# Kernel optimization log

Hardware: AMD Instinct MI355X
Metric: run time of the kernel (lower is better)

## Reference

```python
import jax, jax.numpy as jnp
import numpy as np

DIM = 128        # per-head dim == model width in this module
Q_HEADS = 16
KV_HEADS = 4
WINDOW = 512
BATCH = 4
SEQ = 2048


def setup_inputs() -> dict:
    key = jax.random.key(0)
    k1, k2, k3 = jax.random.split(key, 3)
    x = jax.random.normal(k1, (BATCH, SEQ, DIM), dtype=jnp.float32)
    # fused qkv weight, stored (in, out) so forward is x @ W_qkv
    W_qkv = jax.random.normal(k2, (DIM, (Q_HEADS + 2 * KV_HEADS) * DIM), dtype=jnp.float32) * (DIM ** -0.5)
    W_proj = jax.random.normal(k3, (Q_HEADS * DIM, DIM), dtype=jnp.float32) * ((Q_HEADS * DIM) ** -0.5)
    return {"x": x, "W_qkv": W_qkv, "W_proj": W_proj}


def _gqa_forward(x, W_qkv, W_proj):
    b, s, d = x.shape
    qkv = x @ W_qkv                                    # [b, s, (Hq+2Hkv)*d]
    qkv = qkv.reshape(b, s, Q_HEADS + 2 * KV_HEADS, d).transpose(0, 2, 1, 3)
    q = qkv[:, :Q_HEADS]                               # [b, Hq, s, d]
    k = qkv[:, Q_HEADS:Q_HEADS + KV_HEADS]             # [b, Hkv, s, d]
    v = qkv[:, Q_HEADS + KV_HEADS:]                    # [b, Hkv, s, d]

    # GQA: repeat kv heads to match q heads
    group = Q_HEADS // KV_HEADS
    k = jnp.repeat(k, group, axis=1)                   # [b, Hq, s, d]
    v = jnp.repeat(v, group, axis=1)

    scale = 1.0 / jnp.sqrt(jnp.float32(d))
    scores = jnp.einsum('bhqd,bhkd->bhqk', q, k) * scale   # [b, Hq, s, s]

    q_idx = jnp.arange(s)[:, None]
    kv_idx = jnp.arange(s)[None, :]
    rel = (q_idx - kv_idx).astype(jnp.float32)         # [s, s]
    # per-head ALiBi slope: exp2(-(h+1)*8/Hq), added (sign matches source)
    h = jnp.arange(Q_HEADS, dtype=jnp.float32)
    slopes = jnp.exp2(-((h + 1.0) * 8.0 / Q_HEADS))    # [Hq]
    scores = scores + slopes[None, :, None, None] * rel[None, None, :, :]

    mask = (q_idx >= kv_idx) & ((q_idx - kv_idx) <= WINDOW)
    scores = jnp.where(mask[None, None], scores, -jnp.inf)
    probs = jax.nn.softmax(scores, axis=-1)

    att = jnp.einsum('bhqk,bhkd->bhqd', probs, v)      # [b, Hq, s, d]
    att = att.transpose(0, 2, 1, 3).reshape(b, s, Q_HEADS * d)
    return att @ W_proj                                # [b, s, d]


def reference(x, W_qkv, W_proj):
    return _gqa_forward(x, W_qkv, W_proj)
```

## Files before the change

kernel.cpp:

```cpp
#include <hip/hip_runtime.h>
#include <math.h>

#define DIM_    128
#define QH_     16
#define KVH_    4
#define WIN_    512
#define BATCH_  4
#define SEQ_    2048
#define QKV_LD  3072
#define ATT_LD  2048

#define NX   (BATCH_*SEQ_*DIM_)
#define NWQ  (DIM_*QKV_LD)
#define NWP  (ATT_LD*DIM_)

typedef __attribute__((ext_vector_type(8))) short short8;
typedef __attribute__((ext_vector_type(4))) float f32x4;
typedef unsigned short u16;
typedef unsigned int u32;

__device__ __forceinline__ u16 f2bf(float f) {
    u32 u = __float_as_uint(f);
    u += 0x7fff + ((u >> 16) & 1);
    return (u16)(u >> 16);
}
__device__ __forceinline__ float bf2f(u16 u) {
    return __uint_as_float(((u32)u) << 16);
}
#define MFMA16 __builtin_amdgcn_mfma_f32_16x16x32_bf16

#if __has_builtin(__builtin_amdgcn_exp2f)
#define EXP2F __builtin_amdgcn_exp2f
#else
#define EXP2F exp2f
#endif

__device__ __forceinline__ void gload_lds16(const u16* g, u16* l) {
    __builtin_amdgcn_global_load_lds(
        (const __attribute__((address_space(1))) unsigned int*)(const void*)g,
        (__attribute__((address_space(3))) unsigned int*)(void*)l, 16, 0, 0);
}

__global__ __launch_bounds__(256) void prep(
    const float* __restrict__ x, const float* __restrict__ Wqkv,
    const float* __restrict__ Wproj,
    u16* __restrict__ xh, u16* __restrict__ wth, u16* __restrict__ wpth)
{
    if (blockIdx.x < 1024) {
        const size_t t = (size_t)blockIdx.x * 256 + threadIdx.x;
        float4 v = *(const float4*)(x + 4 * t);
        ushort4 o;
        o.x = f2bf(v.x); o.y = f2bf(v.y); o.z = f2bf(v.z); o.w = f2bf(v.w);
        *(ushort4*)(xh + 4 * t) = o;
        return;
    }
    __shared__ float T[32][33];
    int tile = blockIdx.x - 1024;
    const float* src; u16* dst; int K, N;
    if (tile < 384) { src = Wqkv;  dst = wth;  K = 128;  N = 3072; }
    else { tile -= 384; src = Wproj; dst = wpth; K = 2048; N = 128; }
    const int ntile = N >> 5;
    const int k0 = (tile / ntile) << 5, n0 = (tile % ntile) << 5;
    const int tx = threadIdx.x & 31, ty = threadIdx.x >> 5;
    #pragma unroll
    for (int i = 0; i < 4; ++i)
        T[ty + 8 * i][tx] = src[(size_t)(k0 + ty + 8 * i) * N + n0 + tx];
    __syncthreads();
    #pragma unroll
    for (int i = 0; i < 4; ++i)
        dst[(size_t)(n0 + ty + 8 * i) * K + k0 + tx] = f2bf(T[tx][ty + 8 * i]);
}

__global__ __launch_bounds__(256) void gemm1_mfma(
    const u16* __restrict__ xh, const u16* __restrict__ wth,
    u16* __restrict__ qkvb, u16* __restrict__ vg)
{
    __shared__ u16 Ab[32][512];
    __shared__ u16 Bb[16][512];
    const int bn = blockIdx.x * 64;
    const int bm = blockIdx.y * 128;
    const int tid = threadIdx.x;
    const int wv = tid >> 6, lane = tid & 63;
    const int lr = lane & 15, quad = lane >> 4;
    const int lo = lane & 15, hi = lane >> 4;

    #pragma unroll
    for (int i = 0; i < 12; ++i) {
        const int idx = wv * 12 + i;
        if (idx < 32) {
            const int mt = idx >> 2, s = idx & 3;
            gload_lds16(xh + (size_t)(bm + mt * 16 + lo) * DIM_ + s * 32 + hi * 8,
                        &Ab[idx][0]);
        } else {
            const int j = idx - 32, nt = j >> 2, s = j & 3;
            gload_lds16(wth + (size_t)(bn + nt * 16 + lo) * DIM_ + s * 32 + hi * 8,
                        &Bb[j][0]);
        }
    }
    __syncthreads();

    const int wr = wv >> 1, wc = wv & 1;
    f32x4 acc[4][2] = {};
    if (bn < 2560) {
        #pragma unroll
        for (int s = 0; s < 4; ++s) {
            short8 af[4], bf[2];
            #pragma unroll
            for (int mt = 0; mt < 4; ++mt)
                af[mt] = *(const short8*)&Ab[(wr * 4 + mt) * 4 + s][lane * 8];
            #pragma unroll
            for (int nt = 0; nt < 2; ++nt)
                bf[nt] = *(const short8*)&Bb[(wc * 2 + nt) * 4 + s][lane * 8];
            #pragma unroll
            for (int mt = 0; mt < 4; ++mt)
                #pragma unroll
                for (int nt = 0; nt < 2; ++nt)
                    acc[mt][nt] = MFMA16(bf[nt], af[mt], acc[mt][nt], 0, 0, 0);
        }
        #pragma unroll
        for (int mt = 0; mt < 4; ++mt)
            #pragma unroll
            for (int nt = 0; nt < 2; ++nt) {
                ushort4 o;
                o.x = f2bf(acc[mt][nt][0]); o.y = f2bf(acc[mt][nt][1]);
                o.z = f2bf(acc[mt][nt][2]); o.w = f2bf(acc[mt][nt][3]);
                *(ushort4*)(qkvb
                    + (size_t)(bm + wr * 64 + mt * 16 + lr) * QKV_LD
                    + bn + wc * 32 + nt * 16 + quad * 4) = o;
            }
    } else {
        #pragma unroll
        for (int s = 0; s < 4; ++s) {
            short8 af[4], bf[2];
            #pragma unroll
            for (int mt = 0; mt < 4; ++mt)
                af[mt] = *(const short8*)&Ab[(wr * 4 + mt) * 4 + s][lane * 8];
            #pragma unroll
            for (int nt = 0; nt < 2; ++nt)
                bf[nt] = *(const short8*)&Bb[(wc * 2 + nt) * 4 + s][lane * 8];
            #pragma unroll
            for (int mt = 0; mt < 4; ++mt)
                #pragma unroll
                for (int nt = 0; nt < 2; ++nt)
                    acc[mt][nt] = MFMA16(af[mt], bf[nt], acc[mt][nt], 0, 0, 0);
        }
        #pragma unroll
        for (int mt = 0; mt < 4; ++mt)
            #pragma unroll
            for (int nt = 0; nt < 2; ++nt) {
                const int ncol = bn + wc * 32 + nt * 16 + lr - 2560;
                const int kvh = ncol >> 7, d = ncol & 127;
                const int m0 = bm + wr * 64 + mt * 16 + quad * 4;
                ushort4 o;
                o.x = f2bf(acc[mt][nt][0]); o.y = f2bf(acc[mt][nt][1]);
                o.z = f2bf(acc[mt][nt][2]); o.w = f2bf(acc[mt][nt][3]);
                *(ushort4*)(vg + ((size_t)((m0 >> 11) * KVH_ + kvh) * DIM_ + d)
                            * SEQ_ + (m0 & 2047)) = o;
            }
    }
}

__global__ __launch_bounds__(256) void attn_mfma(
    const u16* __restrict__ qkvb, const u16* __restrict__ vg,
    u16* __restrict__ ah)
{
    const int xcd  = blockIdx.x & 7;
    const int idx  = blockIdx.x >> 3;
    const int pair = xcd + 8 * (idx & 1);
    const int qt   = idx >> 1;
    const int b    = pair >> 2, kvh = pair & 3;
    const int q0 = qt << 5;
    const int tid = threadIdx.x;
    const int wv = tid >> 6, lane = tid & 63;
    const int lr = lane & 15, quad = lane >> 4;
    const int h = kvh * 4 + wv;

    __shared__ u16 Kb[4][8][512];
    __shared__ u16 Vb[4][8][512];
    __shared__ u16 Pt[4][32][36];

    const float scale2 = 0.08838834764831845f * 1.4426950408889634f;
    const float slope2 = exp2f(-0.5f * (float)(h + 1)) * 1.4426950408889634f;
    const int jbase = max(0, q0 - WIN_);
    const int nch = (q0 + 32 - jbase) >> 5;
    const size_t rowb = (size_t)b * SEQ_;
    const u16* kg  = qkvb + rowb * QKV_LD + (QH_ + kvh) * DIM_;
    const u16* vgb = vg + (size_t)(b * KVH_ + kvh) * DIM_ * SEQ_;
    const int lo = lane & 15, hi = lane >> 4;

    short8 qf[2][4];
    #pragma unroll
    for (int m = 0; m < 2; ++m) {
        const u16* qp = qkvb + (rowb + q0 + m * 16 + lr) * QKV_LD
                        + h * DIM_ + quad * 8;
        #pragma unroll
        for (int s = 0; s < 4; ++s) qf[m][s] = *(const short8*)(qp + 32 * s);
    }

    float alpha[2];
    #pragma unroll
    for (int m = 0; m < 2; ++m) {
        const int q = q0 + m * 16 + lr;
        const int rm = (q < WIN_) ? q : WIN_;
        alpha[m] = slope2 * (float)(q - rm);
    }

    f32x4 O[2][8] = {};
    float rs[2] = {0.f, 0.f};

    #define STAGE(CH, SLOT) do {                                              \
        const int _jk = jbase + ((CH) << 5);                                  \
        _Pragma("unroll")                                                     \
        for (int _t = 0; _t < 2; ++_t) {                                      \
            const int _p = wv + _t * 4;                                       \
            gload_lds16(kg + (size_t)(_jk + (_p >> 2) * 16 + lo) * QKV_LD     \
                        + (_p & 3) * 32 + hi * 8, &Kb[(SLOT)][_p][0]);        \
            gload_lds16(vgb + (size_t)(_p * 16 + lo) * SEQ_ + _jk + hi * 8,   \
                        &Vb[(SLOT)][_p][0]);                                  \
        }                                                                     \
    } while (0)

    STAGE(0, 0);
    { const int c1 = (1 < nch) ? 1 : (nch - 1); STAGE(c1, 1); }

    for (int ch = 0; ch < nch; ++ch) {
        const int jk = jbase + (ch << 5);
        const int slot = ch & 3;
        { const int cn = (ch + 2 < nch) ? (ch + 2) : (nch - 1);
          STAGE(cn, (ch + 2) & 3); }
        __asm__ volatile("s_waitcnt vmcnt(8)" ::: "memory");
        __asm__ volatile("s_barrier" ::: "memory");

        #pragma unroll
        for (int nt = 0; nt < 2; ++nt) {
            f32x4 c0 = {0.f, 0.f, 0.f, 0.f}, c1 = {0.f, 0.f, 0.f, 0.f};
            #pragma unroll
            for (int s = 0; s < 4; ++s) {
                short8 kf = *(const short8*)&Kb[slot][nt * 4 + s][lane * 8];
                c0 = MFMA16(kf, qf[0][s], c0, 0, 0, 0);
                c1 = MFMA16(kf, qf[1][s], c1, 0, 0, 0);
            }
            const int jknt = jk + nt * 16;
            #pragma unroll
            for (int m = 0; m < 2; ++m) {
                const f32x4 c = m ? c1 : c0;
                const int qm0 = q0 + m * 16;
                const float b0 = fmaf(-slope2, (float)(jknt + quad * 4), alpha[m]);
                float e0, e1, e2, e3;
                if (qm0 >= jknt + 15 && qm0 + 15 <= jknt + WIN_) {
                    e0 = EXP2F(fmaf(c[0], scale2, b0));
                    e1 = EXP2F(fmaf(c[1], scale2, b0 - slope2));
                    e2 = EXP2F(fmaf(c[2], scale2, b0 - 2.f * slope2));
                    e3 = EXP2F(fmaf(c[3], scale2, b0 - 3.f * slope2));
                } else {
                    const int q = qm0 + lr, j0q = jknt + quad * 4;
                    float ee[4];
                    #pragma unroll
                    for (int r = 0; r < 4; ++r) {
                        const int rel = q - (j0q + r);
                        const float t = fmaf(c[r], scale2, b0 - (float)r * slope2);
                        ee[r] = ((unsigned)rel <= (unsigned)WIN_) ? EXP2F(t) : 0.f;
                    }
                    e0 = ee[0]; e1 = ee[1]; e2 = ee[2]; e3 = ee[3];
                }
                rs[m] += (e0 + e1) + (e2 + e3);
                ushort4 o;
                o.x = f2bf(e0); o.y = f2bf(e1); o.z = f2bf(e2); o.w = f2bf(e3);
                *(ushort4*)&Pt[wv][m * 16 + lr][nt * 16 + quad * 4] = o;
            }
        }
        __asm__ volatile("s_waitcnt lgkmcnt(0)" ::: "memory");

        short8 pa0 = *(const short8*)&Pt[wv][lr][quad * 8];
        short8 pa1 = *(const short8*)&Pt[wv][16 + lr][quad * 8];
        #pragma unroll
        for (int nt = 0; nt < 8; ++nt) {
            short8 vf = *(const short8*)&Vb[slot][nt][lane * 8];
            O[0][nt] = MFMA16(vf, pa0, O[0][nt], 0, 0, 0);
            O[1][nt] = MFMA16(vf, pa1, O[1][nt], 0, 0, 0);
        }
    }
    #undef STAGE

    __asm__ volatile("s_waitcnt vmcnt(0)" ::: "memory");

    #pragma unroll
    for (int m = 0; m < 2; ++m) {
        rs[m] += __shfl_xor(rs[m], 16);
        rs[m] += __shfl_xor(rs[m], 32);
    }

    #pragma unroll
    for (int m = 0; m < 2; ++m) {
        const float inv = 1.0f / rs[m];
        u16* dst = ah + (rowb + q0 + m * 16 + lr) * (size_t)ATT_LD + h * DIM_;
        #pragma unroll
        for (int nt = 0; nt < 8; ++nt) {
            ushort4 o;
            o.x = f2bf(O[m][nt][0] * inv); o.y = f2bf(O[m][nt][1] * inv);
            o.z = f2bf(O[m][nt][2] * inv); o.w = f2bf(O[m][nt][3] * inv);
            *(ushort4*)(dst + nt * 16 + quad * 4) = o;
        }
    }
}

__global__ __launch_bounds__(256) void gemm2_mfma(
    const u16* __restrict__ ah, const u16* __restrict__ wpth,
    float* __restrict__ out)
{
    const int bm = blockIdx.x * 16;
    const int wv = threadIdx.x >> 6, lane = threadIdx.x & 63;
    const int lr = lane & 15, quad = lane >> 4;
    const int cq = wv;

    const u16* arow  = ah + (size_t)(bm + lr) * ATT_LD + quad * 8;
    const u16* w0row = wpth + (size_t)(cq * 32 + lr) * ATT_LD + quad * 8;
    const u16* w1row = w0row + (size_t)16 * ATT_LD;

    f32x4 acc0 = {0.f, 0.f, 0.f, 0.f}, acc1 = {0.f, 0.f, 0.f, 0.f};
    #pragma unroll 8
    for (int k0 = 0; k0 < ATT_LD; k0 += 32) {
        short8 a  = *(const short8*)(arow + k0);
        short8 w0 = *(const short8*)(w0row + k0);
        short8 w1 = *(const short8*)(w1row + k0);
        acc0 = MFMA16(w0, a, acc0, 0, 0, 0);
        acc1 = MFMA16(w1, a, acc1, 0, 0, 0);
    }
    float* orow = out + (size_t)(bm + lr) * DIM_ + cq * 32;
    *(float4*)(orow + quad * 4)      = *(float4*)&acc0;
    *(float4*)(orow + 16 + quad * 4) = *(float4*)&acc1;
}

extern "C" void kernel_launch(void* const* d_in, const int* in_sizes, int n_in,
                              void* d_out, int out_size, void* d_ws, size_t ws_size,
                              hipStream_t stream)
{
    const float* x     = (const float*)d_in[0];
    const float* Wqkv  = (const float*)d_in[1];
    const float* Wproj = (const float*)d_in[2];
    float* out = (float*)d_out;

    u16* xh   = (u16*)d_ws;
    u16* wth  = xh   + (size_t)NX;
    u16* wpth = wth  + (size_t)NWQ;
    u16* qkvb = wpth + (size_t)NWP;
    u16* vg   = qkvb + (size_t)8192 * QKV_LD;
    u16* ahp  = vg   + (size_t)BATCH_ * KVH_ * DIM_ * SEQ_;

    prep<<<1024 + 640, 256, 0, stream>>>(x, Wqkv, Wproj, xh, wth, wpth);

    gemm1_mfma<<<dim3(QKV_LD / 64, 8192 / 128), 256, 0, stream>>>(
        xh, wth, qkvb, vg);

    attn_mfma<<<1024, 256, 0, stream>>>(qkvb, vg, ahp);

    gemm2_mfma<<<8192 / 16, 256, 0, stream>>>(ahp, wpth, out);
}
```

Measured before the change: 202.0 us.

## Halve attention query tile, double-buffer K/V, use packed bf16 conversion

Cuts the attention query tile from 32 to 16 rows per wave and doubles the grid, so there are more blocks and fewer registers and less LDS per block. The K/V pipeline drops from four-slot depth-two prefetch to two-slot depth-one prefetch, adds a second barrier per chunk and clamps the last chunk's load address. Every fp32-to-bf16 conversion in the GEMM epilogue and attention now uses the hardware packed conversion instruction instead of manual rounding. The trade-off is that each K/V chunk is now loaded for only 16 query rows, which doubles K/V traffic, and load latency is less hidden.

```diff
diff --git a/kernel.cpp b/kernel.cpp
--- a/kernel.cpp
+++ b/kernel.cpp
@@ -26,6 +26,11 @@
 }
 __device__ __forceinline__ float bf2f(u16 u) {
     return __uint_as_float(((u32)u) << 16);
+}
+__device__ __forceinline__ u32 pkbf(float a, float b) {
+    u32 r;
+    __asm__("v_cvt_pk_bf16_f32 %0, %1, %2" : "=v"(r) : "v"(a), "v"(b));
+    return r;
 }
 #define MFMA16 __builtin_amdgcn_mfma_f32_16x16x32_bf16
 
@@ -121,10 +126,10 @@
         for (int mt = 0; mt < 4; ++mt)
             #pragma unroll
             for (int nt = 0; nt < 2; ++nt) {
-                ushort4 o;
-                o.x = f2bf(acc[mt][nt][0]); o.y = f2bf(acc[mt][nt][1]);
-                o.z = f2bf(acc[mt][nt][2]); o.w = f2bf(acc[mt][nt][3]);
-                *(ushort4*)(qkvb
+                uint2 o;
+                o.x = pkbf(acc[mt][nt][0], acc[mt][nt][1]);
+                o.y = pkbf(acc[mt][nt][2], acc[mt][nt][3]);
+                *(uint2*)(qkvb
                     + (size_t)(bm + wr * 64 + mt * 16 + lr) * QKV_LD
                     + bn + wc * 32 + nt * 16 + quad * 4) = o;
             }
@@ -151,16 +156,16 @@
                 const int ncol = bn + wc * 32 + nt * 16 + lr - 2560;
                 const int kvh = ncol >> 7, d = ncol & 127;
                 const int m0 = bm + wr * 64 + mt * 16 + quad * 4;
-                ushort4 o;
-                o.x = f2bf(acc[mt][nt][0]); o.y = f2bf(acc[mt][nt][1]);
-                o.z = f2bf(acc[mt][nt][2]); o.w = f2bf(acc[mt][nt][3]);
-                *(ushort4*)(vg + ((size_t)((m0 >> 11) * KVH_ + kvh) * DIM_ + d)
+                uint2 o;
+                o.x = pkbf(acc[mt][nt][0], acc[mt][nt][1]);
+                o.y = pkbf(acc[mt][nt][2], acc[mt][nt][3]);
+                *(uint2*)(vg + ((size_t)((m0 >> 11) * KVH_ + kvh) * DIM_ + d)
                             * SEQ_ + (m0 & 2047)) = o;
             }
     }
 }
 
-__global__ __launch_bounds__(256) void attn_mfma(
+__global__ __launch_bounds__(256, 4) void attn_mfma(
     const u16* __restrict__ qkvb, const u16* __restrict__ vg,
     u16* __restrict__ ah)
 {
@@ -169,47 +174,45 @@
     const int pair = xcd + 8 * (idx & 1);
     const int qt   = idx >> 1;
     const int b    = pair >> 2, kvh = pair & 3;
-    const int q0 = qt << 5;
+    const int q0 = qt << 4;
     const int tid = threadIdx.x;
     const int wv = tid >> 6, lane = tid & 63;
     const int lr = lane & 15, quad = lane >> 4;
     const int h = kvh * 4 + wv;
 
-    __shared__ u16 Kb[4][8][512];
-    __shared__ u16 Vb[4][8][512];
-    __shared__ u16 Pt[4][32][36];
+    __shared__ u16 Kb[2][8][512];
+    __shared__ u16 Vb[2][8][512];
+    __shared__ u16 Pt[4][16][36];
 
     const float scale2 = 0.08838834764831845f * 1.4426950408889634f;
     const float slope2 = exp2f(-0.5f * (float)(h + 1)) * 1.4426950408889634f;
     const int jbase = max(0, q0 - WIN_);
-    const int nch = (q0 + 32 - jbase) >> 5;
+    const int nch = (q0 + 16 - jbase + 31) >> 5;
     const size_t rowb = (size_t)b * SEQ_;
     const u16* kg  = qkvb + rowb * QKV_LD + (QH_ + kvh) * DIM_;
     const u16* vgb = vg + (size_t)(b * KVH_ + kvh) * DIM_ * SEQ_;
     const int lo = lane & 15, hi = lane >> 4;
 
-    short8 qf[2][4];
-    #pragma unroll
-    for (int m = 0; m < 2; ++m) {
-        const u16* qp = qkvb + (rowb + q0 + m * 16 + lr) * QKV_LD
-                        + h * DIM_ + quad * 8;
-        #pragma unroll
-        for (int s = 0; s < 4; ++s) qf[m][s] = *(const short8*)(qp + 32 * s);
-    }
-
-    float alpha[2];
-    #pragma unroll
-    for (int m = 0; m < 2; ++m) {
-        const int q = q0 + m * 16 + lr;
+    short8 qf[4];
+    {
+        const u16* qp = qkvb + (rowb + q0 + lr) * QKV_LD + h * DIM_ + quad * 8;
+        #pragma unroll
+        for (int s = 0; s < 4; ++s) qf[s] = *(const short8*)(qp + 32 * s);
+    }
+
+    float alpha0;
+    {
+        const int q = q0 + lr;
         const int rm = (q < WIN_) ? q : WIN_;
-        alpha[m] = slope2 * (float)(q - rm);
-    }
-
-    f32x4 O[2][8] = {};
-    float rs[2] = {0.f, 0.f};
+        alpha0 = slope2 * (float)(q - rm);
+    }
+
+    f32x4 O[8] = {};
+    float rs = 0.f;
 
     #define STAGE(CH, SLOT) do {                                              \
-        const int _jk = jbase + ((CH) << 5);                                  \
+        const int _jk0 = jbase + ((CH) << 5);                                 \
+        const int _jk = (_jk0 < SEQ_ - 32) ? _jk0 : (SEQ_ - 32);              \
         _Pragma("unroll")                                                     \
         for (int _t = 0; _t < 2; ++_t) {                                      \
             const int _p = wv + _t * 4;                                       \
@@ -221,85 +224,74 @@
     } while (0)
 
     STAGE(0, 0);
-    { const int c1 = (1 < nch) ? 1 : (nch - 1); STAGE(c1, 1); }
 
     for (int ch = 0; ch < nch; ++ch) {
         const int jk = jbase + (ch << 5);
-        const int slot = ch & 3;
-        { const int cn = (ch + 2 < nch) ? (ch + 2) : (nch - 1);
-          STAGE(cn, (ch + 2) & 3); }
-        __asm__ volatile("s_waitcnt vmcnt(8)" ::: "memory");
+        const int slot = ch & 1;
+        { const int cn = (ch + 1 < nch) ? (ch + 1) : (nch - 1);
+          STAGE(cn, slot ^ 1); }
+        __asm__ volatile("s_waitcnt vmcnt(4)" ::: "memory");
         __asm__ volatile("s_barrier" ::: "memory");
 
         #pragma unroll
         for (int nt = 0; nt < 2; ++nt) {
-            f32x4 c0 = {0.f, 0.f, 0.f, 0.f}, c1 = {0.f, 0.f, 0.f, 0.f};
+            f32x4 c0 = {0.f, 0.f, 0.f, 0.f};
             #pragma unroll
             for (int s = 0; s < 4; ++s) {
                 short8 kf = *(const short8*)&Kb[slot][nt * 4 + s][lane * 8];
-                c0 = MFMA16(kf, qf[0][s], c0, 0, 0, 0);
-                c1 = MFMA16(kf, qf[1][s], c1, 0, 0, 0);
+                c0 = MFMA16(kf, qf[s], c0, 0, 0, 0);
             }
             const int jknt = jk + nt * 16;
-            #pragma unroll
-            for (int m = 0; m < 2; ++m) {
-                const f32x4 c = m ? c1 : c0;
-                const int qm0 = q0 + m * 16;
-                const float b0 = fmaf(-slope2, (float)(jknt + quad * 4), alpha[m]);
-                float e0, e1, e2, e3;
-                if (qm0 >= jknt + 15 && qm0 + 15 <= jknt + WIN_) {
-                    e0 = EXP2F(fmaf(c[0], scale2, b0));
-                    e1 = EXP2F(fmaf(c[1], scale2, b0 - slope2));
-                    e2 = EXP2F(fmaf(c[2], scale2, b0 - 2.f * slope2));
-                    e3 = EXP2F(fmaf(c[3], scale2, b0 - 3.f * slope2));
-                } else {
-                    const int q = qm0 + lr, j0q = jknt + quad * 4;
-                    float ee[4];
-                    #pragma unroll
-                    for (int r = 0; r < 4; ++r) {
-                        const int rel = q - (j0q + r);
-                        const float t = fmaf(c[r], scale2, b0 - (float)r * slope2);
-                        ee[r] = ((unsigned)rel <= (unsigned)WIN_) ? EXP2F(t) : 0.f;
-                    }
-                    e0 = ee[0]; e1 = ee[1]; e2 = ee[2]; e3 = ee[3];
+            const float b0 = fmaf(-slope2, (float)(jknt + quad * 4), alpha0);
+            float e0, e1, e2, e3;
+            if (q0 >= jknt + 15 && q0 + 15 <= jknt + WIN_) {
+                e0 = EXP2F(fmaf(c0[0], scale2, b0));
+                e1 = EXP2F(fmaf(c0[1], scale2, b0 - slope2));
+                e2 = EXP2F(fmaf(c0[2], scale2, b0 - 2.f * slope2));
+                e3 = EXP2F(fmaf(c0[3], scale2, b0 - 3.f * slope2));
+            } else {
+                const int q = q0 + lr, j0q = jknt + quad * 4;
+                float ee[4];
+                #pragma unroll
+                for (int r = 0; r < 4; ++r) {
+                    const int rel = q - (j0q + r);
+                    const float t = fmaf(c0[r], scale2, b0 - (float)r * slope2);
+                    ee[r] = ((unsigned)rel <= (unsigned)WIN_) ? EXP2F(t) : 0.f;
                 }
-                rs[m] += (e0 + e1) + (e2 + e3);
-                ushort4 o;
-                o.x = f2bf(e0); o.y = f2bf(e1); o.z = f2bf(e2); o.w = f2bf(e3);
-                *(ushort4*)&Pt[wv][m * 16 + lr][nt * 16 + quad * 4] = o;
+                e0 = ee[0]; e1 = ee[1]; e2 = ee[2]; e3 = ee[3];
             }
+            rs += (e0 + e1) + (e2 + e3);
+            uint2 o;
+            o.x = pkbf(e0, e1);
+            o.y = pkbf(e2, e3);
+            *(uint2*)&Pt[wv][lr][nt * 16 + quad * 4] = o;
         }
         __asm__ volatile("s_waitcnt lgkmcnt(0)" ::: "memory");
 
         short8 pa0 = *(const short8*)&Pt[wv][lr][quad * 8];
-        short8 pa1 = *(const short8*)&Pt[wv][16 + lr][quad * 8];
         #pragma unroll
         for (int nt = 0; nt < 8; ++nt) {
             short8 vf = *(const short8*)&Vb[slot][nt][lane * 8];
-            O[0][nt] = MFMA16(vf, pa0, O[0][nt], 0, 0, 0);
-            O[1][nt] = MFMA16(vf, pa1, O[1][nt], 0, 0, 0);
-        }
+            O[nt] = MFMA16(vf, pa0, O[nt], 0, 0, 0);
+        }
+        __asm__ volatile("s_barrier" ::: "memory");
     }
     #undef STAGE
 
     __asm__ volatile("s_waitcnt vmcnt(0)" ::: "memory");
 
-    #pragma unroll
-    for (int m = 0; m < 2; ++m) {
-        rs[m] += __shfl_xor(rs[m], 16);
-        rs[m] += __shfl_xor(rs[m], 32);
-    }
-
-    #pragma unroll
-    for (int m = 0; m < 2; ++m) {
-        const float inv = 1.0f / rs[m];
-        u16* dst = ah + (rowb + q0 + m * 16 + lr) * (size_t)ATT_LD + h * DIM_;
+    rs += __shfl_xor(rs, 16);
+    rs += __shfl_xor(rs, 32);
+
+    {
+        const float inv = 1.0f / rs;
+        u16* dst = ah + (rowb + q0 + lr) * (size_t)ATT_LD + h * DIM_;
         #pragma unroll
         for (int nt = 0; nt < 8; ++nt) {
-            ushort4 o;
-            o.x = f2bf(O[m][nt][0] * inv); o.y = f2bf(O[m][nt][1] * inv);
-            o.z = f2bf(O[m][nt][2] * inv); o.w = f2bf(O[m][nt][3] * inv);
-            *(ushort4*)(dst + nt * 16 + quad * 4) = o;
+            uint2 o;
+            o.x = pkbf(O[nt][0] * inv, O[nt][1] * inv);
+            o.y = pkbf(O[nt][2] * inv, O[nt][3] * inv);
+            *(uint2*)(dst + nt * 16 + quad * 4) = o;
         }
     }
 }
@@ -352,7 +344,7 @@
     gemm1_mfma<<<dim3(QKV_LD / 64, 8192 / 128), 256, 0, stream>>>(
         xh, wth, qkvb, vg);
 
-    attn_mfma<<<1024, 256, 0, stream>>>(qkvb, vg, ahp);
+    attn_mfma<<<2048, 256, 0, stream>>>(qkvb, vg, ahp);
 
     gemm2_mfma<<<8192 / 16, 256, 0, stream>>>(ahp, wpth, out);
 }
```

New measurement: 212.2 us. +5.0%, slower.
